# Performance work log

Measured on AMD Instinct MI355X. Metric: run time of the kernel, lower is better.

## Reference

```python
import jax, jax.numpy as jnp
import numpy as np

B, S, D_IN, D_OUT = 4, 4096, 2048, 2048
NUM_ADAPTERS, RANK = 8, 16


def setup_inputs() -> dict:
    key = jax.random.key(0)
    ks = jax.random.split(key, 7)
    x = jax.random.normal(ks[0], (B, S, D_IN), dtype=jnp.float32)
    # adapter ids per token in [0, NUM_ADAPTERS]; 0 means 'no adapter'
    lora_mapping = jax.random.randint(ks[1], (B * S,), 0, NUM_ADAPTERS + 1, dtype=jnp.int32)
    weight = jax.random.normal(ks[2], (D_OUT, D_IN), dtype=jnp.float32) * (D_IN ** -0.5)
    bias = jax.random.normal(ks[3], (D_OUT,), dtype=jnp.float32) * 0.01
    # stacked adapters: aid a (1-indexed in mapping) lives at row a-1
    lora_a = jax.random.normal(ks[4], (NUM_ADAPTERS, RANK, D_IN), dtype=jnp.float32) * (D_IN ** -0.5)
    lora_b = jax.random.normal(ks[5], (NUM_ADAPTERS, D_OUT, RANK), dtype=jnp.float32) * (RANK ** -0.5)
    scaling = jnp.full((NUM_ADAPTERS,), 2.0, dtype=jnp.float32)
    return {"x": x, "lora_mapping": lora_mapping, "weight": weight, "bias": bias,
            "lora_a": lora_a, "lora_b": lora_b, "scaling": scaling}


def reference(x, lora_mapping, weight, bias, lora_a, lora_b, scaling):
    # Base dense linear: res = x @ W^T + b
    res = jnp.einsum('bsd,od->bso', x, weight) + bias  # [B,S,D_OUT]
    n_adapters = lora_a.shape[0]
    x2 = x.reshape(-1, x.shape[-1])                    # [N, D_IN]
    # one_hot(aid-1): aid==0 maps to -1 -> all-zero row (adapter skipped),
    # matching the torch loop that ignores aid 0. Fold scaling in here.
    sel = jax.nn.one_hot(lora_mapping - 1, n_adapters, dtype=x.dtype) * scaling  # [N, A]
    # Batched gather-matmul-scatter expressed as dense-over-adapters einsum:
    # u[n,a,r] = x[n] @ la[a]^T ; masked/scaled by sel ; delta[n] = sum_a u[n,a] @ lb[a]^T
    u = jnp.einsum('nd,ard->nar', x2, lora_a) * sel[..., None]  # [N, A, R]
    delta = jnp.einsum('nar,aor->no', u, lora_b)                # [N, D_OUT]
    return res + delta.reshape(res.shape)
```

## Files before the change

kernel.cpp:

```cpp
#include <hip/hip_runtime.h>
#include <hip/hip_bf16.h>


#define D_IN   2048
#define D_OUT  2048
#define NTOK   16384
#define RANK   16
#define NADAPT 8
#define KEXT   2176
#define BM     128
#define BN     128
#define BK     64

typedef __attribute__((ext_vector_type(8))) __bf16 bf16x8;
typedef __attribute__((ext_vector_type(4))) float  f32x4;

__device__ inline unsigned short f2bf(float f) {
    unsigned u = __builtin_bit_cast(unsigned, f);
    u += 0x7fffu + ((u >> 16) & 1u);
    return (unsigned short)(u >> 16);
}

__global__ void prep_x(const float4* __restrict__ x, const int* __restrict__ map,
                       const float4* __restrict__ lora_a, const float* __restrict__ scaling,
                       unsigned short* __restrict__ Xe) {
    int wave = threadIdx.x >> 6, lane = threadIdx.x & 63;
    int n = blockIdx.x * 4 + wave;
    const float4* xr = x + (size_t)n * (D_IN / 4);
    unsigned short* xo = Xe + (size_t)n * KEXT;

    float4 xv[8];
#pragma unroll
    for (int j = 0; j < 8; ++j) {
        xv[j] = xr[j * 64 + lane];
        ushort4 s;
        s.x = f2bf(xv[j].x); s.y = f2bf(xv[j].y);
        s.z = f2bf(xv[j].z); s.w = f2bf(xv[j].w);
        *(ushort4*)(xo + (j * 64 + lane) * 4) = s;
    }

    int aid = map[n];
    int c0 = lane * 2;
    float myu0 = 0.f, myu1 = 0.f;
    int r0 = c0 & 15;
    if (aid > 0) {
        int a = aid - 1;
        float sc = scaling[a];
        const float4* lab = lora_a + (size_t)a * RANK * (D_IN / 4);
#pragma unroll
        for (int r = 0; r < RANK; ++r) {
            const float4* lar = lab + r * (D_IN / 4);
            float acc = 0.f;
#pragma unroll
            for (int j = 0; j < 8; ++j) {
                float4 lv = lar[j * 64 + lane];
                acc += xv[j].x * lv.x + xv[j].y * lv.y + xv[j].z * lv.z + xv[j].w * lv.w;
            }
#pragma unroll
            for (int m = 32; m >= 1; m >>= 1) acc += __shfl_xor(acc, m, 64);
            float uv = acc * sc;
            if (r == r0)     myu0 = uv;
            if (r == r0 + 1) myu1 = uv;
        }
    }
    ushort2 e; e.x = 0; e.y = 0;
    if (aid > 0 && (c0 >> 4) == (aid - 1)) { e.x = f2bf(myu0); e.y = f2bf(myu1); }
    *(ushort2*)(xo + D_IN + c0) = e;
}

__global__ void prep_w(const float4* __restrict__ w, const float* __restrict__ lora_b,
                       unsigned short* __restrict__ We) {
    int wave = threadIdx.x >> 6, lane = threadIdx.x & 63;
    int o = blockIdx.x * 4 + wave;
    const float4* wr = w + (size_t)o * (D_IN / 4);
    unsigned short* wo = We + (size_t)o * KEXT;
#pragma unroll
    for (int j = 0; j < 8; ++j) {
        float4 v = wr[j * 64 + lane];
        ushort4 s;
        s.x = f2bf(v.x); s.y = f2bf(v.y); s.z = f2bf(v.z); s.w = f2bf(v.w);
        *(ushort4*)(wo + (j * 64 + lane) * 4) = s;
    }
    int c0 = lane * 2;
    int a = c0 >> 4, r = c0 & 15;
    const float* src = lora_b + ((size_t)a * D_OUT + o) * RANK + r;
    ushort2 e; e.x = f2bf(src[0]); e.y = f2bf(src[1]);
    *(ushort2*)(wo + D_IN + c0) = e;
}

__global__ void gemm_fused(const unsigned short* __restrict__ Xe,
                           const unsigned short* __restrict__ We,
                           const float* __restrict__ bias,
                           float* __restrict__ out) {
    __shared__ unsigned short As[BM * BK];
    __shared__ unsigned short Bs[BN * BK];

    int t = threadIdx.x;
    int lane = t & 63, wave = t >> 6;
    int g = blockIdx.x;
    int group = g >> 7, within = g & 127;
    int bm = group * 8 + (within & 7);
    int bn = within >> 3;

    int wm = wave >> 1, wn = wave & 1;
    f32x4 acc[4][4] = {};

    for (int k0 = 0; k0 < KEXT; k0 += BK) {
        __syncthreads();
#pragma unroll
        for (int c = 0; c < 4; ++c) {
            int linear = (wave * 4 + c) * 64 + lane;
            int row = linear >> 3;
            int kc  = linear & 7;
            int gc  = kc ^ (row & 7);
            const unsigned short* ga = Xe + (size_t)(bm * BM + row) * KEXT + k0 + gc * 8;
            __builtin_amdgcn_global_load_lds(
                (const __attribute__((address_space(1))) unsigned int*)ga,
                (__attribute__((address_space(3))) unsigned int*)(As + (wave * 4 + c) * 512),
                16, 0, 0);
            const unsigned short* gb = We + (size_t)(bn * BN + row) * KEXT + k0 + gc * 8;
            __builtin_amdgcn_global_load_lds(
                (const __attribute__((address_space(1))) unsigned int*)gb,
                (__attribute__((address_space(3))) unsigned int*)(Bs + (wave * 4 + c) * 512),
                16, 0, 0);
        }
        __syncthreads();
#pragma unroll
        for (int ks = 0; ks < 2; ++ks) {
            bf16x8 af[4], bfr[4];
            int gchunk = ks * 4 + (lane >> 4);
            int sw = gchunk ^ (lane & 7);
#pragma unroll
            for (int i = 0; i < 4; ++i) {
                int rowA = wm * 64 + i * 16 + (lane & 15);
                af[i]  = *(const bf16x8*)(As + rowA * BK + sw * 8);
                int rowB = wn * 64 + i * 16 + (lane & 15);
                bfr[i] = *(const bf16x8*)(Bs + rowB * BK + sw * 8);
            }
#pragma unroll
            for (int i = 0; i < 4; ++i)
#pragma unroll
                for (int j = 0; j < 4; ++j)
                    acc[i][j] = __builtin_amdgcn_mfma_f32_16x16x32_bf16(af[i], bfr[j], acc[i][j], 0, 0, 0);
        }
    }

    int colq = lane & 15, rq = lane >> 4;
#pragma unroll
    for (int j = 0; j < 4; ++j) {
        int col = bn * BN + wn * 64 + j * 16 + colq;
        float bv = bias[col];
#pragma unroll
        for (int i = 0; i < 4; ++i) {
            int row0 = bm * BM + wm * 64 + i * 16 + rq * 4;
#pragma unroll
            for (int r = 0; r < 4; ++r)
                out[(size_t)(row0 + r) * D_OUT + col] = acc[i][j][r] + bv;
        }
    }
}

extern "C" void kernel_launch(void* const* d_in, const int* in_sizes, int n_in,
                              void* d_out, int out_size, void* d_ws, size_t ws_size,
                              hipStream_t stream) {
    (void)in_sizes; (void)n_in; (void)out_size; (void)ws_size;
    const float* x       = (const float*)d_in[0];
    const int*   map     = (const int*)d_in[1];
    const float* weight  = (const float*)d_in[2];
    const float* bias    = (const float*)d_in[3];
    const float* lora_a  = (const float*)d_in[4];
    const float* lora_b  = (const float*)d_in[5];
    const float* scaling = (const float*)d_in[6];
    float* out = (float*)d_out;

    unsigned short* Xe = (unsigned short*)d_ws;
    unsigned short* We = Xe + (size_t)NTOK * KEXT;

    prep_x<<<NTOK / 4, 256, 0, stream>>>((const float4*)x, map, (const float4*)lora_a, scaling, Xe);
    prep_w<<<D_OUT / 4, 256, 0, stream>>>((const float4*)weight, lora_b, We);
    gemm_fused<<<(NTOK / BM) * (D_OUT / BN), 256, 0, stream>>>(Xe, We, bias, out);
}
```

Measured before the change: 462.6 us.

## Compute LoRA down-projection in prep via MFMA over all adapters

Replaces the scalar per-token LoRA-A dot-product loop (16 rank reductions with wave shuffles per token) with a block-level MFMA that computes x·A^T for 16 tokens against all 8 adapters' ranks at once, then masks by adapter id when writing the extended columns. A new small kernel first converts lora_a to bf16 in workspace. This trades the scalar FMA and shuffle work for dense bf16 matrix ops that do 8x redundant adapter work, and it adds a bf16 rounding of x and lora_a before the product. Each block also re-reads x rows for both the conversion copy and the MFMA operand.

```diff
diff --git a/kernel.cpp b/kernel.cpp
--- a/kernel.cpp
+++ b/kernel.cpp
@@ -13,6 +13,7 @@
 #define BK     64
 
 typedef __attribute__((ext_vector_type(8))) __bf16 bf16x8;
+typedef __attribute__((ext_vector_type(8))) unsigned short u16x8;
 typedef __attribute__((ext_vector_type(4))) float  f32x4;
 
 __device__ inline unsigned short f2bf(float f) {
@@ -21,51 +22,65 @@
     return (unsigned short)(u >> 16);
 }
 
-__global__ void prep_x(const float4* __restrict__ x, const int* __restrict__ map,
-                       const float4* __restrict__ lora_a, const float* __restrict__ scaling,
-                       unsigned short* __restrict__ Xe) {
-    int wave = threadIdx.x >> 6, lane = threadIdx.x & 63;
-    int n = blockIdx.x * 4 + wave;
-    const float4* xr = x + (size_t)n * (D_IN / 4);
-    unsigned short* xo = Xe + (size_t)n * KEXT;
+__global__ void conv_la(const float4* __restrict__ la, ushort4* __restrict__ La) {
+    int t = blockIdx.x * 256 + threadIdx.x;
+    float4 v = la[t];
+    ushort4 s;
+    s.x = f2bf(v.x); s.y = f2bf(v.y); s.z = f2bf(v.z); s.w = f2bf(v.w);
+    La[t] = s;
+}
 
-    float4 xv[8];
-#pragma unroll
-    for (int j = 0; j < 8; ++j) {
-        xv[j] = xr[j * 64 + lane];
-        ushort4 s;
-        s.x = f2bf(xv[j].x); s.y = f2bf(xv[j].y);
-        s.z = f2bf(xv[j].z); s.w = f2bf(xv[j].w);
-        *(ushort4*)(xo + (j * 64 + lane) * 4) = s;
+__global__ void prep_x_mfma(const float* __restrict__ x, const int* __restrict__ map,
+                            const unsigned short* __restrict__ La,
+                            const float* __restrict__ scaling,
+                            unsigned short* __restrict__ Xe) {
+    int t = threadIdx.x, lane = t & 63, wave = t >> 6;
+    int n0 = blockIdx.x * 16;
+    int crow = t >> 4;
+    int ckc  = t & 15;
+    int arow = lane & 15;
+    int kq   = lane >> 4;
+
+    f32x4 acc[2] = {};
+
+    const float* xrow_c = x + (size_t)(n0 + crow) * D_IN + ckc * 2;
+    unsigned short* xo_c = Xe + (size_t)(n0 + crow) * KEXT + ckc * 2;
+    const float* xrow_a = x + (size_t)(n0 + arow) * D_IN + kq * 8;
+    const unsigned short* lb0 = La + (size_t)(wave * 32 + arow) * D_IN + kq * 8;
+    const unsigned short* lb1 = lb0 + (size_t)16 * D_IN;
+
+    for (int k0 = 0; k0 < D_IN; k0 += 32) {
+        float2 cv = *(const float2*)(xrow_c + k0);
+        ushort2 cs; cs.x = f2bf(cv.x); cs.y = f2bf(cv.y);
+        *(ushort2*)(xo_c + k0) = cs;
+        float4 a0 = *(const float4*)(xrow_a + k0);
+        float4 a1 = *(const float4*)(xrow_a + k0 + 4);
+        u16x8 au;
+        au[0] = f2bf(a0.x); au[1] = f2bf(a0.y); au[2] = f2bf(a0.z); au[3] = f2bf(a0.w);
+        au[4] = f2bf(a1.x); au[5] = f2bf(a1.y); au[6] = f2bf(a1.z); au[7] = f2bf(a1.w);
+        bf16x8 af = __builtin_bit_cast(bf16x8, au);
+        bf16x8 b0 = *(const bf16x8*)(lb0 + k0);
+        bf16x8 b1 = *(const bf16x8*)(lb1 + k0);
+        acc[0] = __builtin_amdgcn_mfma_f32_16x16x32_bf16(af, b0, acc[0], 0, 0, 0);
+        acc[1] = __builtin_amdgcn_mfma_f32_16x16x32_bf16(af, b1, acc[1], 0, 0, 0);
     }
 
-    int aid = map[n];
-    int c0 = lane * 2;
-    float myu0 = 0.f, myu1 = 0.f;
-    int r0 = c0 & 15;
-    if (aid > 0) {
-        int a = aid - 1;
+    int aid_m[4];
+#pragma unroll
+    for (int r = 0; r < 4; ++r) aid_m[r] = map[n0 + kq * 4 + r];
+#pragma unroll
+    for (int j = 0; j < 2; ++j) {
+        int c = wave * 32 + j * 16 + arow;
+        int a = c >> 4;
         float sc = scaling[a];
-        const float4* lab = lora_a + (size_t)a * RANK * (D_IN / 4);
 #pragma unroll
-        for (int r = 0; r < RANK; ++r) {
-            const float4* lar = lab + r * (D_IN / 4);
-            float acc = 0.f;
-#pragma unroll
-            for (int j = 0; j < 8; ++j) {
-                float4 lv = lar[j * 64 + lane];
-                acc += xv[j].x * lv.x + xv[j].y * lv.y + xv[j].z * lv.z + xv[j].w * lv.w;
-            }
-#pragma unroll
-            for (int m = 32; m >= 1; m >>= 1) acc += __shfl_xor(acc, m, 64);
-            float uv = acc * sc;
-            if (r == r0)     myu0 = uv;
-            if (r == r0 + 1) myu1 = uv;
+        for (int r = 0; r < 4; ++r) {
+            int token = n0 + kq * 4 + r;
+            unsigned short v = 0;
+            if (aid_m[r] == a + 1) v = f2bf(acc[j][r] * sc);
+            Xe[(size_t)token * KEXT + D_IN + c] = v;
         }
     }
-    ushort2 e; e.x = 0; e.y = 0;
-    if (aid > 0 && (c0 >> 4) == (aid - 1)) { e.x = f2bf(myu0); e.y = f2bf(myu1); }
-    *(ushort2*)(xo + D_IN + c0) = e;
 }
 
 __global__ void prep_w(const float4* __restrict__ w, const float* __restrict__ lora_b,
@@ -175,8 +190,10 @@
 
     unsigned short* Xe = (unsigned short*)d_ws;
     unsigned short* We = Xe + (size_t)NTOK * KEXT;
+    unsigned short* La = We + (size_t)D_OUT * KEXT;
 
-    prep_x<<<NTOK / 4, 256, 0, stream>>>((const float4*)x, map, (const float4*)lora_a, scaling, Xe);
+    conv_la<<<256, 256, 0, stream>>>((const float4*)lora_a, (ushort4*)La);
+    prep_x_mfma<<<NTOK / 16, 256, 0, stream>>>(x, map, La, scaling, Xe);
     prep_w<<<D_OUT / 4, 256, 0, stream>>>((const float4*)weight, lora_b, We);
     gemm_fused<<<(NTOK / BM) * (D_OUT / BN), 256, 0, stream>>>(Xe, We, bias, out);
 }
```

After: 456.1 us. Within noise of the previous version (-1.4%).
